# Kernel optimization log

Measured on AMD Instinct MI355X. Metric: run time of the kernel, lower is better.

## Reference

```python
import jax, jax.numpy as jnp
import numpy as np

POOLED_H = 7
POOLED_W = 7
SPATIAL_SCALE = 0.25
SAMPLING = 2  # bilinear samples per bin edge (standard Mask R-CNN setting)


def setup_inputs() -> dict:
    key = jax.random.key(0)
    k1, k2, k3, k4 = jax.random.split(key, 4)
    B, C, H, W = 2, 256, 200, 304
    K = 1024
    IMG_H, IMG_W = 800.0, 1216.0  # input-image coords; feature map = img * spatial_scale
    features = jax.random.normal(k1, (B, C, H, W), dtype=jnp.float32)
    bidx = jax.random.randint(k2, (K,), 0, B).astype(jnp.float32)
    xs = jnp.sort(jax.random.uniform(k3, (K, 2), dtype=jnp.float32) * IMG_W, axis=1)
    ys = jnp.sort(jax.random.uniform(k4, (K, 2), dtype=jnp.float32) * IMG_H, axis=1)
    rois = jnp.stack([bidx, xs[:, 0], ys[:, 0], xs[:, 1], ys[:, 1]], axis=1)  # [K,5]
    return {"features": features, "rois": rois}


def _axis_interp(coord, size):
    # coord: [K, S] continuous sample positions along one axis of length `size`.
    # Returns low/high integer indices and bilinear weights (zeroed outside [-1, size]).
    valid = ((coord >= -1.0) & (coord <= jnp.float32(size))).astype(coord.dtype)
    c = jnp.clip(coord, 0.0, jnp.float32(size - 1))
    lo = jnp.floor(c)
    hi = jnp.minimum(lo + 1.0, jnp.float32(size - 1))
    frac = c - lo
    return lo.astype(jnp.int32), hi.astype(jnp.int32), (1.0 - frac) * valid, frac * valid


def reference(features, rois):
    B, C, H, W = features.shape
    K = rois.shape[0]
    bidx = rois[:, 0].astype(jnp.int32)
    x1 = rois[:, 1] * SPATIAL_SCALE
    y1 = rois[:, 2] * SPATIAL_SCALE
    x2 = rois[:, 3] * SPATIAL_SCALE
    y2 = rois[:, 4] * SPATIAL_SCALE
    roi_w = jnp.maximum(x2 - x1, 1.0)
    roi_h = jnp.maximum(y2 - y1, 1.0)
    bin_w = roi_w / POOLED_W
    bin_h = roi_h / POOLED_H

    # sample coords: y = y1 + ((j + 0.5)/S) * bin_h, j = py*S + iy  -> [K, PH*S]
    jy = (jnp.arange(POOLED_H * SAMPLING, dtype=jnp.float32) + 0.5) / SAMPLING
    jx = (jnp.arange(POOLED_W * SAMPLING, dtype=jnp.float32) + 0.5) / SAMPLING
    ys = y1[:, None] + jy[None, :] * bin_h[:, None]  # [K, Ys]
    xs = x1[:, None] + jx[None, :] * bin_w[:, None]  # [K, Xs]

    ylo, yhi, wy0, wy1 = _axis_interp(ys, H)
    xlo, xhi, wx0, wx1 = _axis_interp(xs, W)

    b = bidx[:, None, None]  # [K,1,1]

    def gather(yi, xi):
        # advanced indexing -> [K, Ys, Xs, C]
        return features[b, :, yi[:, :, None], xi[:, None, :]]

    def wgt(wy, wx):
        return (wy[:, :, None] * wx[:, None, :])[..., None]  # [K,Ys,Xs,1]

    v = (gather(ylo, xlo) * wgt(wy0, wx0)
         + gather(ylo, xhi) * wgt(wy0, wx1)
         + gather(yhi, xlo) * wgt(wy1, wx0)
         + gather(yhi, xhi) * wgt(wy1, wx1))  # [K, Ys, Xs, C]

    # average the SxS samples within each bin
    v = v.reshape(K, POOLED_H, SAMPLING, POOLED_W, SAMPLING, C).mean(axis=(2, 4))
    return jnp.transpose(v, (0, 3, 1, 2))  # [K, C, PH, PW]
```

## Files before the change

kernel.cpp:

```cpp
#include <hip/hip_runtime.h>
#include <hip/hip_fp16.h>

#define CC 256
#define HH 200
#define WW 304
#define PHW 49
#define NCHUNK 4
#define CHC 64
#define SSTR 65
#define TXT 64
#define TSTR 66

struct Interp { int lo, hi; float w0, w1; };

__device__ __forceinline__ Interp axis_interp(float coord, int size) {
  float valid = (coord >= -1.0f && coord <= (float)size) ? 1.0f : 0.0f;
  float c = fminf(fmaxf(coord, 0.0f), (float)(size - 1));
  float fl = floorf(c);
  int lo = (int)fl;
  int hi = min(lo + 1, size - 1);
  float fr = c - fl;
  Interp r;
  r.lo = lo; r.hi = hi;
  r.w0 = (1.0f - fr) * valid;
  r.w1 = fr * valid;
  return r;
}

__global__ __launch_bounds__(1024) void k_sortrois(const float* __restrict__ rois,
                                                   int K, int Bp,
                                                   int* __restrict__ perm) {
  __shared__ int whist[16][32];
  __shared__ int keytot[32];
  __shared__ int keybase[32];
  int tid = threadIdx.x;
  if (K > 1024) {
    for (int i = tid; i < K; i += 1024) perm[i] = i;
    return;
  }
  int wave = tid >> 6, lane = tid & 63;
  bool active = tid < K;
  int key = 63;
  if (active) {
    const float* r = rois + (size_t)tid * 5;
    int b = (int)r[0];
    float cx = (r[1] + r[3]) * 0.125f;
    float cy = (r[2] + r[4]) * 0.125f;
    int rx = (int)(cx * (8.0f / (float)WW)); rx = max(0, min(7, rx));
    int ry = cy >= (float)(HH / 2) ? 1 : 0;
    key = (((b & 1) * 2 + ry) * 8 + rx) & 31;
  }
  if (tid < 512) ((int*)whist)[tid] = 0;
  __syncthreads();
  unsigned long long m = ~0ull;
#pragma unroll
  for (int bit = 0; bit < 6; ++bit) {
    unsigned long long bb = __ballot((key >> bit) & 1);
    m &= ((key >> bit) & 1) ? bb : ~bb;
  }
  unsigned long long below = m & ((1ull << lane) - 1ull);
  int rank = __popcll(below);
  if (active && below == 0ull) whist[wave][key] = __popcll(m);
  __syncthreads();
  if (tid < 32) {
    int total = 0;
    for (int w = 0; w < 16; ++w) {
      int t = whist[w][tid];
      whist[w][tid] = total;
      total += t;
    }
    keytot[tid] = total;
  }
  __syncthreads();
  if (tid == 0) {
    int base = 0;
    for (int k2 = 0; k2 < 32; ++k2) { keybase[k2] = base; base += keytot[k2]; }
  }
  __syncthreads();
  if (active) perm[keybase[key] + whist[wave][key] + rank] = tid;
}

__global__ __launch_bounds__(256) void k_transpose64(const float* __restrict__ src,
                                                     __half* __restrict__ dst,
                                                     int Bp) {
  __shared__ float tile[TXT][TSTR];
  int xq = blockIdx.x;
  int plane = blockIdx.y;
  int chunk = blockIdx.z;
  int b = plane / HH;
  int y = plane - b * HH;
  int x0 = xq * TXT;
  int xlen = min(TXT, WW - x0);
  const float* sp = src + ((size_t)b * CC + chunk * CHC) * (HH * WW) +
                    (size_t)y * WW + x0;
  int ch = threadIdx.x >> 2;
  int xb = (threadIdx.x & 3) * 4;
  const float* srow = sp + (size_t)ch * (HH * WW);
#pragma unroll
  for (int i = 0; i < 4; ++i) {
    int x = xb + i * 16;
    if (x < xlen) {
      float4 v = *(const float4*)(srow + x);
      tile[x + 0][ch] = v.x;
      tile[x + 1][ch] = v.y;
      tile[x + 2][ch] = v.z;
      tile[x + 3][ch] = v.w;
    }
  }
  __syncthreads();
  __half* dp = dst + (((size_t)chunk * Bp + b) * (size_t)(HH * WW) +
                      (size_t)y * WW + x0) * CHC;
  int xr = threadIdx.x >> 3;
  int c8 = (threadIdx.x & 7) * 8;
#pragma unroll
  for (int pass = 0; pass < 2; ++pass) {
    int x = xr + pass * 32;
    if (x < xlen) {
      const float* trow = &tile[x][c8];
      union { uint4 u; __half2 h[4]; } pk;
      pk.h[0] = __floats2half2_rn(trow[0], trow[1]);
      pk.h[1] = __floats2half2_rn(trow[2], trow[3]);
      pk.h[2] = __floats2half2_rn(trow[4], trow[5]);
      pk.h[3] = __floats2half2_rn(trow[6], trow[7]);
      *(uint4*)(dp + (size_t)x * CHC + c8) = pk.u;
    }
  }
}

__global__ __launch_bounds__(512, 8) void k_gather(const __half* __restrict__ feat,
                                                   const float* __restrict__ rois,
                                                   const int* __restrict__ perm,
                                                   float* __restrict__ out,
                                                   int K, int Bp) {
  __shared__ float stage[PHW][SSTR];
  __shared__ int   xoff[14][2];
  __shared__ float xwgt[14][2];
  __shared__ int2  yoff[14];
  __shared__ float2 ywgt[14];
  int q = gridDim.x >> 3;
  int bx = blockIdx.x;
  int slot = (bx & 7) * q + (bx >> 3);
  if (slot >= K) return;
  int k = perm[slot];
  int chunk = blockIdx.y;

  const float* r = rois + (size_t)k * 5;
  int b = __builtin_amdgcn_readfirstlane((int)r[0]);
  float x1 = r[1] * 0.25f, y1 = r[2] * 0.25f;
  float x2 = r[3] * 0.25f, y2 = r[4] * 0.25f;
  float bin_w = fmaxf(x2 - x1, 1.0f) * (1.0f / 7.0f);
  float bin_h = fmaxf(y2 - y1, 1.0f) * (1.0f / 7.0f);

  int tid = threadIdx.x;
  if (tid < 32) {
    int axis = tid >> 4;
    int j = tid & 15;
    if (j < 14) {
      float start = axis ? y1 : x1;
      float binsz = axis ? bin_h : bin_w;
      int size = axis ? HH : WW;
      float coord = start + ((float)j + 0.5f) * 0.5f * binsz;
      Interp ii = axis_interp(coord, size);
      if (axis) {
        yoff[j] = make_int2(ii.lo * (WW * CHC * 2), ii.hi * (WW * CHC * 2));
        ywgt[j] = make_float2(ii.w0, ii.w1);
      } else {
        xoff[j][0] = ii.lo * (CHC * 2);
        xoff[j][1] = ii.hi * (CHC * 2);
        xwgt[j][0] = ii.w0 * 0.25f;
        xwgt[j][1] = ii.w1 * 0.25f;
      }
    }
  }
  __syncthreads();

  int wave = tid >> 6;
  int lane = tid & 63;
  int xsel = lane >> 5;
  int cq = lane & 31;
  const char* fb = (const char*)(feat +
      ((size_t)chunk * Bp + b) * (size_t)(HH * WW) * CHC);
  int laneByte = cq * 4;

  for (int p = wave; p < PHW; p += 8) {
    int ph = p / 7;
    int pw = p - ph * 7;
    int jx0 = 2 * pw, jy0 = 2 * ph;
    int2 yo0 = yoff[jy0], yo1 = yoff[jy0 + 1];
    float2 yw0 = ywgt[jy0], yw1 = ywgt[jy0 + 1];
    __half2 w00 = __float2half2_rn(yw0.x), w01 = __float2half2_rn(yw0.y);
    __half2 w10 = __float2half2_rn(yw1.x), w11 = __float2half2_rn(yw1.y);
    float ax = 0.f, ay = 0.f;
#pragma unroll
    for (int sx = 0; sx < 2; ++sx) {
      int xo = xoff[jx0 + sx][xsel] + laneByte;
      float wx = xwgt[jx0 + sx][xsel];
#pragma unroll
      for (int sy = 0; sy < 2; ++sy) {
        const __half2 wlo = sy ? w10 : w00;
        const __half2 whi = sy ? w11 : w01;
        int2 yo = sy ? yo1 : yo0;
        ushort2 u0 = *(const ushort2*)(fb + (yo.x + xo));
        ushort2 u1 = *(const ushort2*)(fb + (yo.y + xo));
        __half2 t = __hfma2(*(__half2*)&u1, whi, __hmul2(*(__half2*)&u0, wlo));
        float2 f = __half22float2(t);
        ax += wx * f.x;
        ay += wx * f.y;
      }
    }
    ax += __shfl_xor(ax, 32);
    ay += __shfl_xor(ay, 32);
    if (lane < 32) {
      stage[p][cq * 2 + 0] = ax;
      stage[p][cq * 2 + 1] = ay;
    }
  }
  __syncthreads();

  float* outk = out + (size_t)k * CC * PHW + (size_t)chunk * CHC * PHW;
  for (int i = tid; i < CHC * PHW; i += 512) {
    int cc = i / PHW;
    int p = i - cc * PHW;
    outk[i] = stage[p][cc];
  }
}

__global__ __launch_bounds__(256) void k_roialign_direct(const float* __restrict__ fe,
                                                         const float* __restrict__ rois,
                                                         float* __restrict__ out,
                                                         int total) {
  int idx = blockIdx.x * 256 + threadIdx.x;
  if (idx >= total) return;
  int pw = idx % 7;
  int t = idx / 7;
  int ph = t % 7; t /= 7;
  int c = t % CC;
  int k = t / CC;
  const float* r = rois + (size_t)k * 5;
  int b = (int)r[0];
  float x1 = r[1] * 0.25f, y1 = r[2] * 0.25f;
  float x2 = r[3] * 0.25f, y2 = r[4] * 0.25f;
  float bin_w = fmaxf(x2 - x1, 1.0f) * (1.0f / 7.0f);
  float bin_h = fmaxf(y2 - y1, 1.0f) * (1.0f / 7.0f);
  const float* base = fe + ((size_t)b * CC + c) * HH * WW;
  float acc = 0.f;
#pragma unroll
  for (int sy = 0; sy < 2; ++sy) {
    float yy = y1 + ((float)(2 * ph + sy) + 0.5f) * 0.5f * bin_h;
    Interp iy = axis_interp(yy, HH);
#pragma unroll
    for (int sx = 0; sx < 2; ++sx) {
      float xx = x1 + ((float)(2 * pw + sx) + 0.5f) * 0.5f * bin_w;
      Interp ix = axis_interp(xx, WW);
      float v00 = base[(size_t)iy.lo * WW + ix.lo];
      float v01 = base[(size_t)iy.lo * WW + ix.hi];
      float v10 = base[(size_t)iy.hi * WW + ix.lo];
      float v11 = base[(size_t)iy.hi * WW + ix.hi];
      acc += iy.w0 * ix.w0 * v00 + iy.w0 * ix.w1 * v01 +
             iy.w1 * ix.w0 * v10 + iy.w1 * ix.w1 * v11;
    }
  }
  out[idx] = acc * 0.25f;
}

extern "C" void kernel_launch(void* const* d_in, const int* in_sizes, int n_in,
                              void* d_out, int out_size, void* d_ws, size_t ws_size,
                              hipStream_t stream) {
  const float* features = (const float*)d_in[0];
  const float* rois = (const float*)d_in[1];
  float* out = (float*)d_out;
  int B = in_sizes[0] / (CC * HH * WW);
  int K = in_sizes[1] / 5;
  size_t feat_bytes = (size_t)B * HH * WW * CC * sizeof(__half);
  size_t perm_bytes = (size_t)((K + 7) & ~7) * sizeof(int);
  if (ws_size >= feat_bytes + perm_bytes && K <= 1024) {
    __half* feat16 = (__half*)d_ws;
    int* perm = (int*)((char*)d_ws + feat_bytes);
    k_sortrois<<<1, 1024, 0, stream>>>(rois, K, B, perm);
    dim3 tg((WW + TXT - 1) / TXT, B * HH, NCHUNK);
    k_transpose64<<<tg, 256, 0, stream>>>(features, feat16, B);
    int q = (K + 7) / 8;
    dim3 gg(8 * q, NCHUNK);
    k_gather<<<gg, 512, 0, stream>>>(feat16, rois, perm, out, K, B);
  } else {
    int total = K * CC * PHW;
    k_roialign_direct<<<(total + 255) / 256, 256, 0, stream>>>(features, rois, out, total);
  }
}
```

Baseline: 77.59 us.

## Fuse ROI sort into transpose kernel and use nontemporal gather loads

Merges the single-block ROI sorting kernel into the feature transpose kernel by adding an extra grid column (blockIdx.x == 5) whose first block performs the sort with 256 threads handling four ROIs each. This removes one kernel launch and its serialization on the stream. The extra grid column launches many blocks that return immediately. Gather loads also switch to nontemporal 32-bit loads, which may change cache behavior for the reused feature data.

New measurement: 92.77 us. +19.6%, slower.

```diff
diff --git a/kernel.cpp b/kernel.cpp
--- a/kernel.cpp
+++ b/kernel.cpp
@@ -27,63 +27,78 @@
   return r;
 }
 
-__global__ __launch_bounds__(1024) void k_sortrois(const float* __restrict__ rois,
-                                                   int K, int Bp,
-                                                   int* __restrict__ perm) {
+__global__ __launch_bounds__(256) void k_transpose_sort(const float* __restrict__ src,
+                                                        __half* __restrict__ dst,
+                                                        const float* __restrict__ rois,
+                                                        int* __restrict__ perm,
+                                                        int K, int Bp) {
+  __shared__ float tile[TXT][TSTR];
   __shared__ int whist[16][32];
   __shared__ int keytot[32];
   __shared__ int keybase[32];
   int tid = threadIdx.x;
-  if (K > 1024) {
-    for (int i = tid; i < K; i += 1024) perm[i] = i;
+
+  if (blockIdx.x == 5) {
+    if (blockIdx.y != 0 || blockIdx.z != 0) return;
+    int wave = tid >> 6, lane = tid & 63;
+    ((int*)whist)[tid] = 0;
+    ((int*)whist)[tid + 256] = 0;
+    int mykey[4], myrank[4];
+#pragma unroll
+    for (int kk = 0; kk < 4; ++kk) {
+      int g = tid + 256 * kk;
+      int key = 63;
+      if (g < K) {
+        const float* r = rois + (size_t)g * 5;
+        int b = (int)r[0];
+        float cx = (r[1] + r[3]) * 0.125f;
+        float cy = (r[2] + r[4]) * 0.125f;
+        int rx = (int)(cx * (8.0f / (float)WW)); rx = max(0, min(7, rx));
+        int ry = cy >= (float)(HH / 2) ? 1 : 0;
+        key = (((b & 1) * 2 + ry) * 8 + rx) & 31;
+      }
+      mykey[kk] = key;
+    }
+    __syncthreads();
+#pragma unroll
+    for (int kk = 0; kk < 4; ++kk) {
+      int key = mykey[kk];
+      int g = tid + 256 * kk;
+      unsigned long long m = ~0ull;
+#pragma unroll
+      for (int bit = 0; bit < 6; ++bit) {
+        unsigned long long bb = __ballot((key >> bit) & 1);
+        m &= ((key >> bit) & 1) ? bb : ~bb;
+      }
+      unsigned long long below = m & ((1ull << lane) - 1ull);
+      myrank[kk] = __popcll(below);
+      if (g < K && below == 0ull) whist[wave + 4 * kk][key] = __popcll(m);
+    }
+    __syncthreads();
+    if (tid < 32) {
+      int total = 0;
+      for (int w = 0; w < 16; ++w) {
+        int t = whist[w][tid];
+        whist[w][tid] = total;
+        total += t;
+      }
+      keytot[tid] = total;
+    }
+    __syncthreads();
+    if (tid == 0) {
+      int base = 0;
+      for (int k2 = 0; k2 < 32; ++k2) { keybase[k2] = base; base += keytot[k2]; }
+    }
+    __syncthreads();
+#pragma unroll
+    for (int kk = 0; kk < 4; ++kk) {
+      int g = tid + 256 * kk;
+      if (g < K)
+        perm[keybase[mykey[kk]] + whist[wave + 4 * kk][mykey[kk]] + myrank[kk]] = g;
+    }
     return;
   }
-  int wave = tid >> 6, lane = tid & 63;
-  bool active = tid < K;
-  int key = 63;
-  if (active) {
-    const float* r = rois + (size_t)tid * 5;
-    int b = (int)r[0];
-    float cx = (r[1] + r[3]) * 0.125f;
-    float cy = (r[2] + r[4]) * 0.125f;
-    int rx = (int)(cx * (8.0f / (float)WW)); rx = max(0, min(7, rx));
-    int ry = cy >= (float)(HH / 2) ? 1 : 0;
-    key = (((b & 1) * 2 + ry) * 8 + rx) & 31;
-  }
-  if (tid < 512) ((int*)whist)[tid] = 0;
-  __syncthreads();
-  unsigned long long m = ~0ull;
-#pragma unroll
-  for (int bit = 0; bit < 6; ++bit) {
-    unsigned long long bb = __ballot((key >> bit) & 1);
-    m &= ((key >> bit) & 1) ? bb : ~bb;
-  }
-  unsigned long long below = m & ((1ull << lane) - 1ull);
-  int rank = __popcll(below);
-  if (active && below == 0ull) whist[wave][key] = __popcll(m);
-  __syncthreads();
-  if (tid < 32) {
-    int total = 0;
-    for (int w = 0; w < 16; ++w) {
-      int t = whist[w][tid];
-      whist[w][tid] = total;
-      total += t;
-    }
-    keytot[tid] = total;
-  }
-  __syncthreads();
-  if (tid == 0) {
-    int base = 0;
-    for (int k2 = 0; k2 < 32; ++k2) { keybase[k2] = base; base += keytot[k2]; }
-  }
-  __syncthreads();
-  if (active) perm[keybase[key] + whist[wave][key] + rank] = tid;
-}
-
-__global__ __launch_bounds__(256) void k_transpose64(const float* __restrict__ src,
-                                                     __half* __restrict__ dst,
-                                                     int Bp) {
-  __shared__ float tile[TXT][TSTR];
+
   int xq = blockIdx.x;
   int plane = blockIdx.y;
   int chunk = blockIdx.z;
@@ -93,8 +108,8 @@
   int xlen = min(TXT, WW - x0);
   const float* sp = src + ((size_t)b * CC + chunk * CHC) * (HH * WW) +
                     (size_t)y * WW + x0;
-  int ch = threadIdx.x >> 2;
-  int xb = (threadIdx.x & 3) * 4;
+  int ch = tid >> 2;
+  int xb = (tid & 3) * 4;
   const float* srow = sp + (size_t)ch * (HH * WW);
 #pragma unroll
   for (int i = 0; i < 4; ++i) {
@@ -110,8 +125,8 @@
   __syncthreads();
   __half* dp = dst + (((size_t)chunk * Bp + b) * (size_t)(HH * WW) +
                       (size_t)y * WW + x0) * CHC;
-  int xr = threadIdx.x >> 3;
-  int c8 = (threadIdx.x & 7) * 8;
+  int xr = tid >> 3;
+  int c8 = (tid & 7) * 8;
 #pragma unroll
   for (int pass = 0; pass < 2; ++pass) {
     int x = xr + pass * 32;
@@ -200,9 +215,9 @@
         const __half2 wlo = sy ? w10 : w00;
         const __half2 whi = sy ? w11 : w01;
         int2 yo = sy ? yo1 : yo0;
-        ushort2 u0 = *(const ushort2*)(fb + (yo.x + xo));
-        ushort2 u1 = *(const ushort2*)(fb + (yo.y + xo));
-        __half2 t = __hfma2(*(__half2*)&u1, whi, __hmul2(*(__half2*)&u0, wlo));
+        int i0 = __builtin_nontemporal_load((const int*)(fb + (yo.x + xo)));
+        int i1 = __builtin_nontemporal_load((const int*)(fb + (yo.y + xo)));
+        __half2 t = __hfma2(*(__half2*)&i1, whi, __hmul2(*(__half2*)&i0, wlo));
         float2 f = __half22float2(t);
         ax += wx * f.x;
         ay += wx * f.y;
@@ -276,9 +291,8 @@
   if (ws_size >= feat_bytes + perm_bytes && K <= 1024) {
     __half* feat16 = (__half*)d_ws;
     int* perm = (int*)((char*)d_ws + feat_bytes);
-    k_sortrois<<<1, 1024, 0, stream>>>(rois, K, B, perm);
-    dim3 tg((WW + TXT - 1) / TXT, B * HH, NCHUNK);
-    k_transpose64<<<tg, 256, 0, stream>>>(features, feat16, B);
+    dim3 tg(6, B * HH, NCHUNK);
+    k_transpose_sort<<<tg, 256, 0, stream>>>(features, feat16, rois, perm, K, B);
     int q = (K + 7) / 8;
     dim3 gg(8 * q, NCHUNK);
     k_gather<<<gg, 512, 0, stream>>>(feat16, rois, perm, out, K, B);
```
